# Kernel tuning notes

Hardware: AMD Instinct MI355X
Metric: run time of the kernel (lower is better)

Reference implementation:

```python
import jax, jax.numpy as jnp
import numpy as np

B, N, C, K, D, H = 4, 16000, 128, 16, 4, 512
EPS = 1e-5


def _bn(x, g, b, m, v):
    # eval-mode BatchNorm1d over channel dim (applied to flattened B*N rows)
    return (x - m) * jax.lax.rsqrt(v + EPS) * g + b


def _ffn(x, W1, b1, W2, g, b, m, v):
    h = jax.nn.gelu(jnp.einsum('bnc,ch->bnh', x, W1) + b1)
    y = jnp.einsum('bnh,hc->bnc', h, W2)  # second linear has no bias
    return _bn(y, g, b, m, v)


def _vector_feature(x, knn):
    # knn edge max-pooling: max_k ( x[b, knn[b,n,k], :] - x[b, n, :] )
    gathered = jnp.take_along_axis(x[:, :, None, :], knn[:, :, :, None], axis=1)  # (B,N,K,C)
    return jnp.max(gathered - x[:, :, None, :], axis=2)


def _vfr(x, knn, W, g, b, m, v):
    y = jnp.einsum('bnc,cd->bnd', x, W)
    y = _vector_feature(y, knn)
    return _bn(y, g, b, m, v)


def setup_inputs():
    key = jax.random.key(0)
    ks = jax.random.split(key, 16)
    s = 0.05
    return {
        'x': jax.random.normal(ks[0], (B, N, C), jnp.float32),
        'pe': jax.random.normal(ks[1], (B, N, C), jnp.float32),
        'knn': jax.random.randint(ks[2], (B, N, K), 0, N, dtype=jnp.int32),
        # mlp (the single leading FFN)
        'mlp_W1': jax.random.normal(ks[3], (C, H), jnp.float32) * s,
        'mlp_b1': jnp.zeros((H,), jnp.float32),
        'mlp_W2': jax.random.normal(ks[4], (H, C), jnp.float32) * s,
        'mlp_g': jax.random.uniform(ks[5], (C,), jnp.float32, 0.5, 1.5),
        'mlp_beta': jnp.zeros((C,), jnp.float32),
        'mlp_m': jnp.zeros((C,), jnp.float32),
        'mlp_v': jnp.ones((C,), jnp.float32),
        # per-depth VFR params (stacked over depth D)
        'vfr_W': jax.random.normal(ks[6], (D, C, C), jnp.float32) * s,
        'vfr_g': jax.random.uniform(ks[7], (D, C), jnp.float32, 0.5, 1.5),
        'vfr_beta': jnp.zeros((D, C), jnp.float32),
        'vfr_m': jnp.zeros((D, C), jnp.float32),
        'vfr_v': jnp.ones((D, C), jnp.float32),
        # per-depth FFN params
        'ffn_W1': jax.random.normal(ks[8], (D, C, H), jnp.float32) * s,
        'ffn_b1': jnp.zeros((D, H), jnp.float32),
        'ffn_W2': jax.random.normal(ks[9], (D, H, C), jnp.float32) * s,
        'ffn_g': jax.random.uniform(ks[10], (D, C), jnp.float32, 0.5, 1.5),
        'ffn_beta': jnp.zeros((D, C), jnp.float32),
        'ffn_m': jnp.zeros((D, C), jnp.float32),
        'ffn_v': jnp.ones((D, C), jnp.float32),
    }


def reference(x, pe, knn,
              mlp_W1, mlp_b1, mlp_W2, mlp_g, mlp_beta, mlp_m, mlp_v,
              vfr_W, vfr_g, vfr_beta, vfr_m, vfr_v,
              ffn_W1, ffn_b1, ffn_W2, ffn_g, ffn_beta, ffn_m, ffn_v):
    # drop_path is identity in eval mode
    x = x + _ffn(x, mlp_W1, mlp_b1, mlp_W2, mlp_g, mlp_beta, mlp_m, mlp_v)
    for i in range(D):
        x = x + pe
        x = x + _vfr(x, knn, vfr_W[i], vfr_g[i], vfr_beta[i], vfr_m[i], vfr_v[i])
        x = x + _ffn(x, ffn_W1[i], ffn_b1[i], ffn_W2[i], ffn_g[i], ffn_beta[i], ffn_m[i], ffn_v[i])
    return x
```

## Files before the change

### kernel.cpp

```cpp
#include <hip/hip_runtime.h>
#include <hip/hip_bf16.h>

typedef __attribute__((ext_vector_type(8))) short bf16x8;
typedef __attribute__((ext_vector_type(4))) short bf16x4;
typedef __attribute__((ext_vector_type(4))) float f32x4;

#define B_ 4
#define N_ 16000
#define C_ 128
#define K_ 16
#define D_ 4
#define H_ 512
#define R_ (B_*N_)
#define EPSV 1e-5f

__device__ __forceinline__ ushort f2bf(float f) {
    uint32_t b = __builtin_bit_cast(uint32_t, f);
    b += 0x7fffu + ((b >> 16) & 1u);
    return (ushort)(b >> 16);
}
__device__ __forceinline__ float bf2f(ushort u) {
    return __builtin_bit_cast(float, (uint32_t)u << 16);
}
__device__ __forceinline__ uint pk2bf(float lo, float hi) {
    return (uint)f2bf(lo) | ((uint)f2bf(hi) << 16);
}
__device__ __forceinline__ float gelu_fast(float v) {
    float v2 = v * v;
    float u = v * fmaf(0.0356774081f, v2, 0.7978845608f);
    float e = __expf(-2.0f * u);
    return v * __builtin_amdgcn_rcpf(1.0f + e);
}
__device__ __forceinline__ void gll16(const void* g, void* l) {
    __builtin_amdgcn_global_load_lds(
        (__attribute__((address_space(1))) void*)g,
        (__attribute__((address_space(3))) void*)l, 16, 0, 0);
}

__global__ void prep_kernel(
    const float* __restrict__ mlp_W1, const float* __restrict__ mlp_b1,
    const float* __restrict__ mlp_W2, const float* __restrict__ mlp_g,
    const float* __restrict__ mlp_be, const float* __restrict__ mlp_m,
    const float* __restrict__ mlp_v,
    const float* __restrict__ vfr_W, const float* __restrict__ vfr_g,
    const float* __restrict__ vfr_be, const float* __restrict__ vfr_m,
    const float* __restrict__ vfr_v,
    const float* __restrict__ ffn_W1, const float* __restrict__ ffn_b1,
    const float* __restrict__ ffn_W2, const float* __restrict__ ffn_g,
    const float* __restrict__ ffn_be, const float* __restrict__ ffn_m,
    const float* __restrict__ ffn_v,
    ushort* __restrict__ w1t, ushort* __restrict__ w2p, ushort* __restrict__ wvs,
    float* __restrict__ b1a, float* __restrict__ fs, float* __restrict__ fb,
    float* __restrict__ vs, float* __restrict__ vb)
{
    int i = blockIdx.x * 256 + threadIdx.x;
    const int NW = 5 * H_ * C_;
    if (i < NW) {
        int f = i / (H_*C_), e = i % (H_*C_);
        int h = e / C_, c = e % C_;
        const float* src = (f == 0) ? mlp_W1 : ffn_W1 + (size_t)(f-1)*C_*H_;
        w1t[i] = f2bf(src[(size_t)c*H_ + h]);
        return;
    }
    i -= NW;
    if (i < NW) {
        int f = i / (H_*C_), e = i % (H_*C_);
        int c = e / H_, p = e % H_;
        int s = p & 31, lam = s >> 3, j = s & 7;
        int h = (p & ~31) + lam*4 + (j & 3) + ((j >> 2) << 4);
        const float* src = (f == 0) ? mlp_W2 : ffn_W2 + (size_t)(f-1)*H_*C_;
        w2p[i] = f2bf(src[(size_t)h*C_ + c]);
        return;
    }
    i -= NW;
    if (i < D_*C_*C_) {
        int d = i / (C_*C_), e = i % (C_*C_);
        int co = e / C_, p = e % C_;
        int s = p & 31, lam = s >> 3, j = s & 7;
        int k = (p & ~31) + lam*4 + (j & 3) + ((j >> 2) << 4);
        wvs[i] = f2bf(vfr_W[(size_t)d*C_*C_ + (size_t)k*C_ + co]);
        return;
    }
    i -= D_*C_*C_;
    if (i < 5*H_) {
        int f = i / H_, h = i % H_;
        b1a[i] = (f == 0) ? mlp_b1[h] : ffn_b1[(f-1)*H_ + h];
        return;
    }
    i -= 5*H_;
    if (i < 5*C_) {
        int f = i / C_, c = i % C_;
        float g  = (f==0) ? mlp_g[c]  : ffn_g[(f-1)*C_ + c];
        float be = (f==0) ? mlp_be[c] : ffn_be[(f-1)*C_ + c];
        float m  = (f==0) ? mlp_m[c]  : ffn_m[(f-1)*C_ + c];
        float v  = (f==0) ? mlp_v[c]  : ffn_v[(f-1)*C_ + c];
        float s = g * rsqrtf(v + EPSV);
        fs[i] = s; fb[i] = be - m * s;
        return;
    }
    i -= 5*C_;
    if (i < D_*C_) {
        float s = vfr_g[i] * rsqrtf(vfr_v[i] + EPSV);
        vs[i] = s; vb[i] = vfr_be[i] - vfr_m[i] * s;
    }
}

template<bool ADD_PE, bool NEXT_T>
__global__ __launch_bounds__(256, 5) void ffn_kernel(
    const float* __restrict__ xin, float* __restrict__ xout,
    const float* __restrict__ pe,
    const ushort* __restrict__ W1t,
    const ushort* __restrict__ W2p,
    const float* __restrict__ b1,
    const float* __restrict__ bns, const float* __restrict__ bnb,
    const ushort* __restrict__ Wvs,
    ushort* __restrict__ tout)
{
    __shared__ __attribute__((aligned(16))) char lds[32768];

    const int tid  = threadIdx.x;
    const int m0   = blockIdx.x * 64;
    const int wv   = tid >> 6;
    const int lane = tid & 63;
    const int lr   = lane & 15;
    const int lh   = lane >> 4;

    auto stageW = [&](int hc, int buf) {
        char* base = lds + buf * 16384;
        const int h0 = hc * 32;
        #pragma unroll
        for (int i = 0; i < 2; ++i) {
            int row = i*16 + wv*4 + (lane >> 4);
            const char* src = (const char*)(W1t + (size_t)(h0 + row) * C_)
                            + (((lane & 15) * 16) ^ ((row & 7) << 4));
            gll16(src, base + i*4096 + wv*1024);
        }
        #pragma unroll
        for (int i = 0; i < 2; ++i) {
            int c = i*64 + wv*16 + (lane >> 2);
            const char* src = (const char*)(W2p + (size_t)c * H_ + h0)
                            + (((lane & 3) * 16) ^ ((c & 3) << 4));
            gll16(src, base + 8192 + i*4096 + wv*1024);
        }
    };
    auto stageWv = [&](int r0, int r1) {
        #pragma unroll
        for (int i = 0; i < 8; ++i) {
            if (i < r0 || i >= r1) continue;
            int r = i*16 + wv*4 + (lane >> 4);
            const char* src = (const char*)(Wvs + (size_t)r * C_)
                            + (((lane & 15) * 16) ^ ((r & 7) << 4));
            gll16(src, lds + i*4096 + wv*1024);
        }
    };

    stageW(0, 0);

    bf16x8 xa[4];
    {
        const float* xrow = xin + (size_t)(m0 + wv*16 + lr) * C_ + lh*8;
        #pragma unroll
        for (int kk = 0; kk < 4; ++kk) {
            float4 v0 = *(const float4*)(xrow + kk*32);
            float4 v1 = *(const float4*)(xrow + kk*32 + 4);
            uint p0 = pk2bf(v0.x, v0.y), p1 = pk2bf(v0.z, v0.w);
            uint p2 = pk2bf(v1.x, v1.y), p3 = pk2bf(v1.z, v1.w);
            uint4 u = {p0, p1, p2, p3};
            xa[kk] = __builtin_bit_cast(bf16x8, u);
        }
    }

    f32x4 acc2[8];
    #pragma unroll
    for (int i = 0; i < 8; ++i) acc2[i] = (f32x4){0.f,0.f,0.f,0.f};

    #pragma unroll 1
    for (int hc = 0; hc < 16; ++hc) {
        const int h0  = hc * 32;
        const int buf = hc & 1;

        float4 biasv[2];
        #pragma unroll
        for (int nf = 0; nf < 2; ++nf)
            biasv[nf] = *(const float4*)(b1 + h0 + nf*16 + lh*4);
        __builtin_amdgcn_sched_barrier(0);

        if (hc < 15) {
            stageW(hc + 1, buf ^ 1);
            asm volatile("s_waitcnt vmcnt(6)" ::: "memory");
        } else if (NEXT_T) {
            stageWv(0, 4);
            asm volatile("s_waitcnt vmcnt(6)" ::: "memory");
        } else {
            asm volatile("s_waitcnt vmcnt(2)" ::: "memory");
        }
        __builtin_amdgcn_s_barrier();
        __builtin_amdgcn_sched_barrier(0);

        char* W1s = lds + buf * 16384;
        char* W2s = W1s + 8192;

        f32x4 acc1[2];
        #pragma unroll
        for (int i = 0; i < 2; ++i) acc1[i] = (f32x4){0.f,0.f,0.f,0.f};
        #pragma unroll
        for (int kk = 0; kk < 4; ++kk) {
            int kb = kk*64 + lh*16;
            #pragma unroll
            for (int nf = 0; nf < 2; ++nf) {
                int rb = nf*16 + lr;
                bf16x8 w1 = *(bf16x8*)(W1s + rb*256 + (kb ^ ((rb&7)<<4)));
                acc1[nf] = __builtin_amdgcn_mfma_f32_16x16x32_bf16(
                    w1, xa[kk], acc1[nf], 0, 0, 0);
            }
        }
        bf16x4 pa[2];
        #pragma unroll
        for (int nf = 0; nf < 2; ++nf) {
            uint q0 = pk2bf(gelu_fast(acc1[nf][0] + biasv[nf].x),
                            gelu_fast(acc1[nf][1] + biasv[nf].y));
            uint q1 = pk2bf(gelu_fast(acc1[nf][2] + biasv[nf].z),
                            gelu_fast(acc1[nf][3] + biasv[nf].w));
            uint2 u = {q0, q1};
            pa[nf] = __builtin_bit_cast(bf16x4, u);
        }
        {
            bf16x8 af = __builtin_shufflevector(pa[0], pa[1], 0,1,2,3,4,5,6,7);
            #pragma unroll
            for (int nf = 0; nf < 8; ++nf) {
                int rb = nf*16 + lr;
                bf16x8 w2 = *(bf16x8*)(W2s + rb*64 + ((lh*16) ^ ((rb&3)<<4)));
                acc2[nf] = __builtin_amdgcn_mfma_f32_16x16x32_bf16(
                    w2, af, acc2[nf], 0, 0, 0);
            }
        }

        __builtin_amdgcn_sched_barrier(0);
        asm volatile("s_waitcnt lgkmcnt(0)" ::: "memory");
        __builtin_amdgcn_s_barrier();
    }

    if (NEXT_T) {
        stageWv(4, 8);
    }

    const int row = m0 + wv*16 + lr;
    bf16x4 pa2[8];
    #pragma unroll
    for (int nf = 0; nf < 8; ++nf) {
        int c0 = nf*16 + lh*4;
        float4 sv = *(const float4*)(bns + c0);
        float4 bv = *(const float4*)(bnb + c0);
        float4 xi = *(const float4*)(xin + (size_t)row * C_ + c0);
        if (ADD_PE) {
            float4 pv = *(const float4*)(pe + (size_t)row * C_ + c0);
            xi.x += pv.x; xi.y += pv.y; xi.z += pv.z; xi.w += pv.w;
        }
        float4 xo;
        xo.x = xi.x + acc2[nf][0] * sv.x + bv.x;
        xo.y = xi.y + acc2[nf][1] * sv.y + bv.y;
        xo.z = xi.z + acc2[nf][2] * sv.z + bv.z;
        xo.w = xi.w + acc2[nf][3] * sv.w + bv.w;
        *(float4*)(xout + (size_t)row * C_ + c0) = xo;
        if (NEXT_T) {
            uint2 u = {pk2bf(xo.x, xo.y), pk2bf(xo.z, xo.w)};
            pa2[nf] = __builtin_bit_cast(bf16x4, u);
        }
    }

    if (NEXT_T) {
        asm volatile("s_waitcnt vmcnt(0)" ::: "memory");
        __builtin_amdgcn_s_barrier();
        __builtin_amdgcn_sched_barrier(0);
        f32x4 acc3[8];
        #pragma unroll
        for (int i = 0; i < 8; ++i) acc3[i] = (f32x4){0.f,0.f,0.f,0.f};
        #pragma unroll
        for (int g = 0; g < 4; ++g) {
            bf16x8 af = __builtin_shufflevector(pa2[2*g], pa2[2*g+1],
                                                0,1,2,3,4,5,6,7);
            int kb = g*64 + lh*16;
            #pragma unroll
            for (int nf = 0; nf < 8; ++nf) {
                int rb = nf*16 + lr;
                bf16x8 wvf = *(bf16x8*)(lds + rb*256 + (kb ^ ((rb&7)<<4)));
                acc3[nf] = __builtin_amdgcn_mfma_f32_16x16x32_bf16(
                    af, wvf, acc3[nf], 0, 0, 0);
            }
        }
        #pragma unroll
        for (int nf = 0; nf < 8; ++nf) {
            int col = nf*16 + lr;
            #pragma unroll
            for (int j = 0; j < 4; ++j) {
                int trow = m0 + wv*16 + lh*4 + j;
                tout[(size_t)trow * C_ + col] = f2bf(acc3[nf][j]);
            }
        }
    }
}

__global__ __launch_bounds__(256) void vfr_gather_kernel(
    float* __restrict__ x, const ushort* __restrict__ t,
    const int* __restrict__ knn,
    const float* __restrict__ s, const float* __restrict__ bb)
{
    const int wv   = threadIdx.x >> 6;
    const int lane = threadIdx.x & 63;
    const int p = blockIdx.x * 4 + wv;
    const int b = p / N_;
    const int base = b * N_;
    const int* kp = knn + (size_t)p * K_;
    const uint* trow = (const uint*)t;

    uint cen = trow[(size_t)p * 64 + lane];
    float c0 = bf2f((ushort)(cen & 0xffffu));
    float c1 = bf2f((ushort)(cen >> 16));
    float m0v = -INFINITY, m1v = -INFINITY;
    #pragma unroll
    for (int k = 0; k < K_; ++k) {
        int idx = kp[k];
        uint g = trow[(size_t)(base + idx) * 64 + lane];
        m0v = fmaxf(m0v, bf2f((ushort)(g & 0xffffu)));
        m1v = fmaxf(m1v, bf2f((ushort)(g >> 16)));
    }
    m0v -= c0; m1v -= c1;

    int c = lane * 2;
    float2 sv = *(const float2*)(s + c);
    float2 bv = *(const float2*)(bb + c);
    size_t o = (size_t)p * C_ + c;
    float2 xv = *(const float2*)(x + o);
    xv.x += m0v * sv.x + bv.x;
    xv.y += m1v * sv.y + bv.y;
    *(float2*)(x + o) = xv;
}

extern "C" void kernel_launch(void* const* d_in, const int* in_sizes, int n_in,
                              void* d_out, int out_size, void* d_ws, size_t ws_size,
                              hipStream_t stream) {
    const float* x      = (const float*)d_in[0];
    const float* pe     = (const float*)d_in[1];
    const int*   knn    = (const int*)d_in[2];
    const float* mlp_W1 = (const float*)d_in[3];
    const float* mlp_b1 = (const float*)d_in[4];
    const float* mlp_W2 = (const float*)d_in[5];
    const float* mlp_g  = (const float*)d_in[6];
    const float* mlp_be = (const float*)d_in[7];
    const float* mlp_m  = (const float*)d_in[8];
    const float* mlp_v  = (const float*)d_in[9];
    const float* vfr_W  = (const float*)d_in[10];
    const float* vfr_g  = (const float*)d_in[11];
    const float* vfr_be = (const float*)d_in[12];
    const float* vfr_m  = (const float*)d_in[13];
    const float* vfr_v  = (const float*)d_in[14];
    const float* ffn_W1 = (const float*)d_in[15];
    const float* ffn_b1 = (const float*)d_in[16];
    const float* ffn_W2 = (const float*)d_in[17];
    const float* ffn_g  = (const float*)d_in[18];
    const float* ffn_be = (const float*)d_in[19];
    const float* ffn_m  = (const float*)d_in[20];
    const float* ffn_v  = (const float*)d_in[21];
    float* out = (float*)d_out;

    char* ws = (char*)d_ws;
    ushort* tbuf = (ushort*)ws;  ws += (size_t)R_ * C_ * 2;
    ushort* w1t  = (ushort*)ws;  ws += (size_t)5 * H_ * C_ * 2;
    ushort* w2p  = (ushort*)ws;  ws += (size_t)5 * C_ * H_ * 2;
    ushort* wvs  = (ushort*)ws;  ws += (size_t)D_ * C_ * C_ * 2;
    float*  b1a  = (float*)ws;   ws += (size_t)5 * H_ * 4;
    float*  fs   = (float*)ws;   ws += (size_t)5 * C_ * 4;
    float*  fb   = (float*)ws;   ws += (size_t)5 * C_ * 4;
    float*  vs   = (float*)ws;   ws += (size_t)D_ * C_ * 4;
    float*  vb   = (float*)ws;   ws += (size_t)D_ * C_ * 4;

    const int prep_items = 2*(5*H_*C_) + D_*C_*C_ + 5*H_ + 5*C_ + D_*C_;
    prep_kernel<<<(prep_items + 255) / 256, 256, 0, stream>>>(
        mlp_W1, mlp_b1, mlp_W2, mlp_g, mlp_be, mlp_m, mlp_v,
        vfr_W, vfr_g, vfr_be, vfr_m, vfr_v,
        ffn_W1, ffn_b1, ffn_W2, ffn_g, ffn_be, ffn_m, ffn_v,
        w1t, w2p, wvs, b1a, fs, fb, vs, vb);

    ffn_kernel<true, true><<<R_/64, 256, 0, stream>>>(
        x, out, pe, w1t, w2p, b1a, fs, fb, wvs, tbuf);

    for (int d = 0; d < D_; ++d) {
        vfr_gather_kernel<<<R_/4, 256, 0, stream>>>(
            out, tbuf, knn, vs + d * C_, vb + d * C_);
        if (d < D_ - 1) {
            ffn_kernel<true, true><<<R_/64, 256, 0, stream>>>(
                out, out, pe,
                w1t + (size_t)(d+1) * H_ * C_, w2p + (size_t)(d+1) * C_ * H_,
                b1a + (d+1) * H_, fs + (d+1) * C_, fb + (d+1) * C_,
                wvs + (size_t)(d+1) * C_ * C_, tbuf);
        } else {
            ffn_kernel<false, false><<<R_/64, 256, 0, stream>>>(
                out, out, pe,
                w1t + (size_t)(d+1) * H_ * C_, w2p + (size_t)(d+1) * C_ * H_,
                b1a + (d+1) * H_, fs + (d+1) * C_, fb + (d+1) * C_,
                wvs, tbuf);
        }
    }
}
```

Measured before the change: 365.8 us.

## Stage FFN input/output and VFR projection through LDS for coalesced global access

Loads x and pe once per block with coalesced row-major float4 accesses, keeps x+pe in registers, and builds the bf16 A fragments via a swizzled LDS tile instead of strided per-lane global loads. The epilogue writes BN output to LDS and then performs coalesced residual updates. The next-layer VFR projection now uses a plain transposed weight loaded in two halves and writes t through LDS in 16-byte rows rather than scattered 2-byte stores. Occupancy hint is lowered from 5 to 3 blocks per CU to allow more registers for the held base values, at the cost of extra barriers and less latency hiding.

New measurement: 423.0 us. +15.6%, slower.

```diff
diff --git a/kernel.cpp b/kernel.cpp
--- a/kernel.cpp
+++ b/kernel.cpp
@@ -49,7 +49,7 @@
     const float* __restrict__ ffn_W2, const float* __restrict__ ffn_g,
     const float* __restrict__ ffn_be, const float* __restrict__ ffn_m,
     const float* __restrict__ ffn_v,
-    ushort* __restrict__ w1t, ushort* __restrict__ w2p, ushort* __restrict__ wvs,
+    ushort* __restrict__ w1t, ushort* __restrict__ w2p, ushort* __restrict__ wvt,
     float* __restrict__ b1a, float* __restrict__ fs, float* __restrict__ fb,
     float* __restrict__ vs, float* __restrict__ vb)
 {
@@ -75,10 +75,8 @@
     i -= NW;
     if (i < D_*C_*C_) {
         int d = i / (C_*C_), e = i % (C_*C_);
-        int co = e / C_, p = e % C_;
-        int s = p & 31, lam = s >> 3, j = s & 7;
-        int k = (p & ~31) + lam*4 + (j & 3) + ((j >> 2) << 4);
-        wvs[i] = f2bf(vfr_W[(size_t)d*C_*C_ + (size_t)k*C_ + co]);
+        int co = e / C_, k = e % C_;
+        wvt[i] = f2bf(vfr_W[(size_t)d*C_*C_ + (size_t)k*C_ + co]);
         return;
     }
     i -= D_*C_*C_;
@@ -106,14 +104,14 @@
 }
 
 template<bool ADD_PE, bool NEXT_T>
-__global__ __launch_bounds__(256, 5) void ffn_kernel(
+__global__ __launch_bounds__(256, 3) void ffn_kernel(
     const float* __restrict__ xin, float* __restrict__ xout,
     const float* __restrict__ pe,
     const ushort* __restrict__ W1t,
     const ushort* __restrict__ W2p,
     const float* __restrict__ b1,
     const float* __restrict__ bns, const float* __restrict__ bnb,
-    const ushort* __restrict__ Wvs,
+    const ushort* __restrict__ Wvt,
     ushort* __restrict__ tout)
 {
     __shared__ __attribute__((aligned(16))) char lds[32768];
@@ -124,6 +122,8 @@
     const int lane = tid & 63;
     const int lr   = lane & 15;
     const int lh   = lane >> 4;
+    const int crow = tid >> 5;
+    const int ccol = (tid & 31) * 4;
 
     auto stageW = [&](int hc, int buf) {
         char* base = lds + buf * 16384;
@@ -143,32 +143,43 @@
             gll16(src, base + 8192 + i*4096 + wv*1024);
         }
     };
-    auto stageWv = [&](int r0, int r1) {
-        #pragma unroll
-        for (int i = 0; i < 8; ++i) {
-            if (i < r0 || i >= r1) continue;
+    auto stageWvHalf = [&](int h) {
+        #pragma unroll
+        for (int i = 0; i < 4; ++i) {
             int r = i*16 + wv*4 + (lane >> 4);
-            const char* src = (const char*)(Wvs + (size_t)r * C_)
+            const char* src = (const char*)(Wvt + (size_t)(h*64 + r) * C_)
                             + (((lane & 15) * 16) ^ ((r & 7) << 4));
-            gll16(src, lds + i*4096 + wv*1024);
+            gll16(src, lds + 16384 + i*4096 + wv*1024);
         }
     };
 
-    stageW(0, 0);
+    float4 base[8];
+    #pragma unroll
+    for (int s = 0; s < 8; ++s) {
+        int row = s*8 + crow;
+        size_t go = (size_t)(m0 + row) * C_ + ccol;
+        float4 xv = *(const float4*)(xin + go);
+        float4 bp = xv;
+        if (ADD_PE) {
+            float4 pv = *(const float4*)(pe + go);
+            bp.x += pv.x; bp.y += pv.y; bp.z += pv.z; bp.w += pv.w;
+        }
+        base[s] = bp;
+        uint2 u = { pk2bf(xv.x, xv.y), pk2bf(xv.z, xv.w) };
+        *(uint2*)(lds + row*256 + ((ccol*2) ^ ((row&7)<<4))) = u;
+    }
+    __syncthreads();
 
     bf16x8 xa[4];
     {
-        const float* xrow = xin + (size_t)(m0 + wv*16 + lr) * C_ + lh*8;
-        #pragma unroll
-        for (int kk = 0; kk < 4; ++kk) {
-            float4 v0 = *(const float4*)(xrow + kk*32);
-            float4 v1 = *(const float4*)(xrow + kk*32 + 4);
-            uint p0 = pk2bf(v0.x, v0.y), p1 = pk2bf(v0.z, v0.w);
-            uint p2 = pk2bf(v1.x, v1.y), p3 = pk2bf(v1.z, v1.w);
-            uint4 u = {p0, p1, p2, p3};
-            xa[kk] = __builtin_bit_cast(bf16x8, u);
-        }
-    }
+        const int arow = wv*16 + lr;
+        #pragma unroll
+        for (int kk = 0; kk < 4; ++kk)
+            xa[kk] = *(bf16x8*)(lds + arow*256 + ((kk*64 + lh*16) ^ ((arow&7)<<4)));
+    }
+    __syncthreads();
+
+    stageW(0, 0);
 
     f32x4 acc2[8];
     #pragma unroll
@@ -187,9 +198,6 @@
 
         if (hc < 15) {
             stageW(hc + 1, buf ^ 1);
-            asm volatile("s_waitcnt vmcnt(6)" ::: "memory");
-        } else if (NEXT_T) {
-            stageWv(0, 4);
             asm volatile("s_waitcnt vmcnt(6)" ::: "memory");
         } else {
             asm volatile("s_waitcnt vmcnt(2)" ::: "memory");
@@ -240,63 +248,100 @@
         __builtin_amdgcn_s_barrier();
     }
 
-    if (NEXT_T) {
-        stageWv(4, 8);
-    }
-
-    const int row = m0 + wv*16 + lr;
-    bf16x4 pa2[8];
+    {
+        const int yrow = wv*16 + lr;
+        #pragma unroll
+        for (int nf = 0; nf < 8; ++nf) {
+            int c0 = nf*16 + lh*4;
+            float4 sv = *(const float4*)(bns + c0);
+            float4 bv = *(const float4*)(bnb + c0);
+            f32x4 yv;
+            yv[0] = acc2[nf][0] * sv.x + bv.x;
+            yv[1] = acc2[nf][1] * sv.y + bv.y;
+            yv[2] = acc2[nf][2] * sv.z + bv.z;
+            yv[3] = acc2[nf][3] * sv.w + bv.w;
+            *(f32x4*)(lds + yrow*512 + ((nf*64 + lh*16) ^ ((yrow&7)<<4))) = yv;
+        }
+    }
+    __syncthreads();
+
+    #pragma unroll
+    for (int s = 0; s < 8; ++s) {
+        int row = s*8 + crow;
+        f32x4 yv = *(f32x4*)(lds + row*512 + ((ccol*4) ^ ((row&7)<<4)));
+        float4 xo;
+        xo.x = base[s].x + yv[0];
+        xo.y = base[s].y + yv[1];
+        xo.z = base[s].z + yv[2];
+        xo.w = base[s].w + yv[3];
+        *(float4*)(xout + (size_t)(m0 + row) * C_ + ccol) = xo;
+        base[s] = xo;
+    }
+    if (!NEXT_T) return;
+
+    __syncthreads();
+
+    #pragma unroll
+    for (int s = 0; s < 8; ++s) {
+        int row = s*8 + crow;
+        uint2 u = { pk2bf(base[s].x, base[s].y), pk2bf(base[s].z, base[s].w) };
+        *(uint2*)(lds + row*256 + ((ccol*2) ^ ((row&7)<<4))) = u;
+    }
+    stageWvHalf(0);
+    __syncthreads();
+
+    bf16x8 af3[4];
+    {
+        const int arow = wv*16 + lr;
+        #pragma unroll
+        for (int g = 0; g < 4; ++g)
+            af3[g] = *(bf16x8*)(lds + arow*256 + ((g*64 + lh*16) ^ ((arow&7)<<4)));
+    }
+    f32x4 acc3[8];
+    #pragma unroll
+    for (int i = 0; i < 8; ++i) acc3[i] = (f32x4){0.f,0.f,0.f,0.f};
+    #pragma unroll
+    for (int g = 0; g < 4; ++g) {
+        int kb = g*64 + lh*16;
+        #pragma unroll
+        for (int nf = 0; nf < 4; ++nf) {
+            int rb = nf*16 + lr;
+            bf16x8 wvf = *(bf16x8*)(lds + 16384 + rb*256 + (kb ^ ((rb&7)<<4)));
+            acc3[nf] = __builtin_amdgcn_mfma_f32_16x16x32_bf16(
+                af3[g], wvf, acc3[nf], 0, 0, 0);
+        }
+    }
+    __syncthreads();
+    stageWvHalf(1);
+    __syncthreads();
+    #pragma unroll
+    for (int g = 0; g < 4; ++g) {
+        int kb = g*64 + lh*16;
+        #pragma unroll
+        for (int nf = 4; nf < 8; ++nf) {
+            int rb = (nf-4)*16 + lr;
+            bf16x8 wvf = *(bf16x8*)(lds + 16384 + rb*256 + (kb ^ ((rb&7)<<4)));
+            acc3[nf] = __builtin_amdgcn_mfma_f32_16x16x32_bf16(
+                af3[g], wvf, acc3[nf], 0, 0, 0);
+        }
+    }
+
     #pragma unroll
     for (int nf = 0; nf < 8; ++nf) {
-        int c0 = nf*16 + lh*4;
-        float4 sv = *(const float4*)(bns + c0);
-        float4 bv = *(const float4*)(bnb + c0);
-        float4 xi = *(const float4*)(xin + (size_t)row * C_ + c0);
-        if (ADD_PE) {
-            float4 pv = *(const float4*)(pe + (size_t)row * C_ + c0);
-            xi.x += pv.x; xi.y += pv.y; xi.z += pv.z; xi.w += pv.w;
-        }
-        float4 xo;
-        xo.x = xi.x + acc2[nf][0] * sv.x + bv.x;
-        xo.y = xi.y + acc2[nf][1] * sv.y + bv.y;
-        xo.z = xi.z + acc2[nf][2] * sv.z + bv.z;
-        xo.w = xi.w + acc2[nf][3] * sv.w + bv.w;
-        *(float4*)(xout + (size_t)row * C_ + c0) = xo;
-        if (NEXT_T) {
-            uint2 u = {pk2bf(xo.x, xo.y), pk2bf(xo.z, xo.w)};
-            pa2[nf] = __builtin_bit_cast(bf16x4, u);
-        }
-    }
-
-    if (NEXT_T) {
-        asm volatile("s_waitcnt vmcnt(0)" ::: "memory");
-        __builtin_amdgcn_s_barrier();
-        __builtin_amdgcn_sched_barrier(0);
-        f32x4 acc3[8];
-        #pragma unroll
-        for (int i = 0; i < 8; ++i) acc3[i] = (f32x4){0.f,0.f,0.f,0.f};
-        #pragma unroll
-        for (int g = 0; g < 4; ++g) {
-            bf16x8 af = __builtin_shufflevector(pa2[2*g], pa2[2*g+1],
-                                                0,1,2,3,4,5,6,7);
-            int kb = g*64 + lh*16;
-            #pragma unroll
-            for (int nf = 0; nf < 8; ++nf) {
-                int rb = nf*16 + lr;
-                bf16x8 wvf = *(bf16x8*)(lds + rb*256 + (kb ^ ((rb&7)<<4)));
-                acc3[nf] = __builtin_amdgcn_mfma_f32_16x16x32_bf16(
-                    af, wvf, acc3[nf], 0, 0, 0);
-            }
-        }
-        #pragma unroll
-        for (int nf = 0; nf < 8; ++nf) {
-            int col = nf*16 + lr;
-            #pragma unroll
-            for (int j = 0; j < 4; ++j) {
-                int trow = m0 + wv*16 + lh*4 + j;
-                tout[(size_t)trow * C_ + col] = f2bf(acc3[nf][j]);
-            }
-        }
+        int col = nf*16 + lr;
+        #pragma unroll
+        for (int j = 0; j < 4; ++j) {
+            int trow = wv*16 + lh*4 + j;
+            *(ushort*)(lds + trow*256 + ((col*2) ^ ((trow&7)<<4))) = f2bf(acc3[nf][j]);
+        }
+    }
+    __syncthreads();
+    #pragma unroll
+    for (int s = 0; s < 4; ++s) {
+        int trow = s*16 + (tid >> 4);
+        int tb   = (tid & 15) * 16;
+        uint4 v = *(uint4*)(lds + trow*256 + (tb ^ ((trow&7)<<4)));
+        *(uint4*)((char*)(tout + (size_t)(m0 + trow) * C_) + tb) = v;
     }
 }
 
@@ -367,7 +412,7 @@
     ushort* tbuf = (ushort*)ws;  ws += (size_t)R_ * C_ * 2;
     ushort* w1t  = (ushort*)ws;  ws += (size_t)5 * H_ * C_ * 2;
     ushort* w2p  = (ushort*)ws;  ws += (size_t)5 * C_ * H_ * 2;
-    ushort* wvs  = (ushort*)ws;  ws += (size_t)D_ * C_ * C_ * 2;
+    ushort* wvt  = (ushort*)ws;  ws += (size_t)D_ * C_ * C_ * 2;
     float*  b1a  = (float*)ws;   ws += (size_t)5 * H_ * 4;
     float*  fs   = (float*)ws;   ws += (size_t)5 * C_ * 4;
     float*  fb   = (float*)ws;   ws += (size_t)5 * C_ * 4;
@@ -379,10 +424,10 @@
         mlp_W1, mlp_b1, mlp_W2, mlp_g, mlp_be, mlp_m, mlp_v,
         vfr_W, vfr_g, vfr_be, vfr_m, vfr_v,
         ffn_W1, ffn_b1, ffn_W2, ffn_g, ffn_be, ffn_m, ffn_v,
-        w1t, w2p, wvs, b1a, fs, fb, vs, vb);
+        w1t, w2p, wvt, b1a, fs, fb, vs, vb);
 
     ffn_kernel<true, true><<<R_/64, 256, 0, stream>>>(
-        x, out, pe, w1t, w2p, b1a, fs, fb, wvs, tbuf);
+        x, out, pe, w1t, w2p, b1a, fs, fb, wvt, tbuf);
 
     for (int d = 0; d < D_; ++d) {
         vfr_gather_kernel<<<R_/4, 256, 0, stream>>>(
@@ -392,13 +437,13 @@
                 out, out, pe,
                 w1t + (size_t)(d+1) * H_ * C_, w2p + (size_t)(d+1) * C_ * H_,
                 b1a + (d+1) * H_, fs + (d+1) * C_, fb + (d+1) * C_,
-                wvs + (size_t)(d+1) * C_ * C_, tbuf);
+                wvt + (size_t)(d+1) * C_ * C_, tbuf);
         } else {
             ffn_kernel<false, false><<<R_/64, 256, 0, stream>>>(
                 out, out, pe,
                 w1t + (size_t)(d+1) * H_ * C_, w2p + (size_t)(d+1) * C_ * H_,
                 b1a + (d+1) * H_, fs + (d+1) * C_, fb + (d+1) * C_,
-                wvs, tbuf);
-        }
-    }
-}
+                wvt, tbuf);
+        }
+    }
+}
```
